# Kernel tuning notes

Measured on AMD Instinct MI355X. Metric: run time of the kernel, lower is better.

Reference implementation:

```python
import jax, jax.numpy as jnp
import numpy as np

B, A, C = 1, 196416, 90
H = W = 1024
SCORE_THRESHOLD = 0.05
MAX_DETECTIONS = 100
# RetinaNet-style BBoxTransform normalization (mean=0, std=[0.1,0.1,0.2,0.2])
STD = (0.1, 0.1, 0.2, 0.2)


def setup_inputs() -> dict:
    key = jax.random.key(0)
    k1, k2, k3, k4, k5, k6, k7 = jax.random.split(key, 7)
    x = jax.random.normal(k1, (B, 3, H, W), dtype=jnp.float32)
    regression = jax.random.normal(k2, (B, A, 4), dtype=jnp.float32) * 0.1
    classification = jax.random.normal(k3, (B, A, C), dtype=jnp.float32)
    # valid anchor boxes (x1, y1, x2, y2)
    cx = jax.random.uniform(k4, (B, A), minval=0.0, maxval=float(W))
    cy = jax.random.uniform(k5, (B, A), minval=0.0, maxval=float(H))
    aw = jax.random.uniform(k6, (B, A), minval=16.0, maxval=256.0)
    ah = jax.random.uniform(k7, (B, A), minval=16.0, maxval=256.0)
    anchors = jnp.stack([cx - 0.5 * aw, cy - 0.5 * ah, cx + 0.5 * aw, cy + 0.5 * ah], axis=2).astype(jnp.float32)
    return {"x": x, "regression": regression, "classification": classification, "anchors": anchors}


def _decode_clip(anchors, regression, img_h, img_w):
    # BBoxTransform: deltas (dx, dy, dw, dh) scaled by std, applied to anchor center/size
    wa = anchors[..., 2] - anchors[..., 0]
    ha = anchors[..., 3] - anchors[..., 1]
    cxa = anchors[..., 0] + 0.5 * wa
    cya = anchors[..., 1] + 0.5 * ha
    dx = regression[..., 0] * STD[0]
    dy = regression[..., 1] * STD[1]
    dw = regression[..., 2] * STD[2]
    dh = regression[..., 3] * STD[3]
    cx = cxa + dx * wa
    cy = cya + dy * ha
    w = jnp.exp(dw) * wa
    h = jnp.exp(dh) * ha
    # ClipBoxes: x1,y1 clamped at 0; x2,y2 clamped at image width/height
    x1 = jnp.maximum(cx - 0.5 * w, 0.0)
    y1 = jnp.maximum(cy - 0.5 * h, 0.0)
    x2 = jnp.minimum(cx + 0.5 * w, float(img_w))
    y2 = jnp.minimum(cy + 0.5 * h, float(img_h))
    return jnp.stack([x1, y1, x2, y2], axis=2)  # [B, A, 4]


def reference(x, regression, classification, anchors):
    img_h, img_w = x.shape[2], x.shape[3]
    boxes = _decode_clip(anchors, regression, img_h, img_w)  # [1, A, 4]
    probs = jax.nn.sigmoid(classification)                    # [1, A, C]
    scores = jnp.max(probs, axis=2)                           # [1, A]
    classes = jnp.argmax(probs, axis=2)                       # [1, A]
    valid_scores = jnp.where(scores > SCORE_THRESHOLD, scores, 0.0)
    vb = boxes[0]            # [A, 4]
    vc = classes[0]          # [A]
    vs = valid_scores[0]     # [A]
    k = min(MAX_DETECTIONS, vs.shape[0])
    _, top_idx = jax.lax.top_k(vs, k)
    final_boxes = vb[top_idx]
    final_scores = vs[top_idx]
    final_classes = vc[top_idx]
    return (final_boxes, final_scores, final_classes)
```

## Files before the change

### kernel.cpp

```cpp
#include <hip/hip_runtime.h>
#include <cmath>

#define A_CNT 196416
#define C_CNT 90
#define QUADS (A_CNT / 4)
#define QITERS (QUADS / 8)
#define TOPK 100u
#define CAPB 2048
#define NB_RED 1536
#define NB_GAT 192

#define OFF_HIST1 785664u
#define OFF_CTRL  789760u
#define OFF_CANDA 789824u
#define OFF_CANDB 790336u

#define AGENT_LD(p)    __hip_atomic_load((p), __ATOMIC_RELAXED, __HIP_MEMORY_SCOPE_AGENT)
#define AGENT_ST(p, v) __hip_atomic_store((p), (v), __ATOMIC_RELAXED, __HIP_MEMORY_SCOPE_AGENT)

__global__ __launch_bounds__(256, 4) void k_reduce(const float* __restrict__ cls,
                                                   unsigned* __restrict__ keys,
                                                   unsigned* __restrict__ hist1,
                                                   unsigned* __restrict__ ctrl) {
    __shared__ unsigned lhist[576];
    __shared__ unsigned sdata[256];
    __shared__ unsigned sbin[2];
    __shared__ int sflag;
    const int t = threadIdx.x;
    for (int j = t; j < 576; j += 256) lhist[j] = 0u;
    __syncthreads();

    const int lane = t & 63;
    const int g = lane >> 3, s = lane & 7;
    const int wid = blockIdx.x * 4 + (t >> 6);
    const float4* __restrict__ cls4 = (const float4*)cls;

    if (wid < QITERS) {
        const int q = wid * 8 + g;
        const float4* __restrict__ r4 = cls4 + (size_t)q * 90;
        float4 v[12];
#pragma unroll
        for (int i = 0; i < 12; ++i) {
            const int j = s + 8 * i;
            v[i] = r4[(j < 90) ? j : 89];
        }
        float m0 = -INFINITY, m1 = -INFINITY, m2 = -INFINITY, m3 = -INFINITY;
#pragma unroll
        for (int i = 0; i < 12; ++i) {
            const int j = s + 8 * i;
            const float4 vv = v[i];
            const float a01 = fmaxf(vv.x, vv.y), a23 = fmaxf(vv.z, vv.w);
            const float all = fmaxf(a01, a23);
            if (j < 22)       m0 = fmaxf(m0, all);
            else if (j == 22) { m0 = fmaxf(m0, a01); m1 = fmaxf(m1, a23); }
            else if (j < 45)  m1 = fmaxf(m1, all);
            else if (j < 67)  m2 = fmaxf(m2, all);
            else if (j == 67) { m2 = fmaxf(m2, a01); m3 = fmaxf(m3, a23); }
            else if (j < 90)  m3 = fmaxf(m3, all);
        }
#pragma unroll
        for (int d = 1; d < 8; d <<= 1) {
            m0 = fmaxf(m0, __shfl_xor(m0, d));
            m1 = fmaxf(m1, __shfl_xor(m1, d));
            m2 = fmaxf(m2, __shfl_xor(m2, d));
            m3 = fmaxf(m3, __shfl_xor(m3, d));
        }
        if (s == 0) {
            float p0 = 1.0f / (1.0f + expf(-m0));
            float p1 = 1.0f / (1.0f + expf(-m1));
            float p2 = 1.0f / (1.0f + expf(-m2));
            float p3 = 1.0f / (1.0f + expf(-m3));
            unsigned k0 = (p0 > 0.05f) ? __float_as_uint(p0) : 0u;
            unsigned k1 = (p1 > 0.05f) ? __float_as_uint(p1) : 0u;
            unsigned k2 = (p2 > 0.05f) ? __float_as_uint(p2) : 0u;
            unsigned k3 = (p3 > 0.05f) ? __float_as_uint(p3) : 0u;
            *(uint4*)(keys + 4 * (size_t)q) = make_uint4(k0, k1, k2, k3);
            unsigned h0 = k0 ? (min(k0 >> 16, 0x3F80u) - 0x3D4Bu) : 0u;
            unsigned h1 = k1 ? (min(k1 >> 16, 0x3F80u) - 0x3D4Bu) : 0u;
            unsigned h2 = k2 ? (min(k2 >> 16, 0x3F80u) - 0x3D4Bu) : 0u;
            unsigned h3 = k3 ? (min(k3 >> 16, 0x3F80u) - 0x3D4Bu) : 0u;
            atomicAdd(&lhist[h0], 1u);
            atomicAdd(&lhist[h1], 1u);
            atomicAdd(&lhist[h2], 1u);
            atomicAdd(&lhist[h3], 1u);
        }
    }
    __syncthreads();
    for (int j = t; j < 576; j += 256) {
        unsigned c = lhist[j];
        if (c) atomicAdd(&hist1[j], c);
    }
    __syncthreads();
    if (t == 0) sflag = (atomicAdd(&ctrl[8], 1u) == NB_RED - 1u) ? 1 : 0;
    __syncthreads();
    if (!sflag) return;

    const unsigned target = TOPK;
    unsigned ssum = 0;
#pragma unroll
    for (int j = 0; j < 4; ++j) ssum += AGENT_LD(&hist1[t * 4 + j]);
    sdata[t] = ssum;
    for (int d = 1; d < 256; d <<= 1) {
        __syncthreads();
        unsigned add = (t + d < 256) ? sdata[t + d] : 0u;
        __syncthreads();
        sdata[t] += add;
    }
    __syncthreads();
    {
        unsigned mysuf  = sdata[t];
        unsigned nxtsuf = (t < 255) ? sdata[t + 1] : 0u;
        if (nxtsuf < target && mysuf >= target) { sbin[0] = (unsigned)t; sbin[1] = nxtsuf; }
    }
    __syncthreads();
    const unsigned chunkB = sbin[0];
    const unsigned gAbove = sbin[1];
    unsigned v = (t < 4) ? AGENT_LD(&hist1[chunkB * 4 + t]) : 0u;
    sdata[t] = v;
    for (int d = 1; d < 256; d <<= 1) {
        __syncthreads();
        unsigned add = (t + d < 256) ? sdata[t + d] : 0u;
        __syncthreads();
        sdata[t] += add;
    }
    __syncthreads();
    {
        unsigned mysuf  = sdata[t] + gAbove;
        unsigned nxtsuf = ((t < 255) ? sdata[t + 1] : 0u) + gAbove;
        if (nxtsuf < target && mysuf >= target) {
            unsigned bin = chunkB * 4 + (unsigned)t;
            ctrl[0] = bin ? (bin + 0x3D4Bu) : 0u;
            ctrl[1] = nxtsuf;
        }
    }
}

__global__ __launch_bounds__(256) void k_gather(const float* __restrict__ cls,
                                                const float* __restrict__ reg,
                                                const float* __restrict__ anc,
                                                const unsigned* __restrict__ keys,
                                                unsigned* __restrict__ ctrl,
                                                unsigned* __restrict__ candA,
                                                unsigned* __restrict__ candB,
                                                float* __restrict__ out) {
    __shared__ unsigned sAi[128], sAk[128];
    __shared__ unsigned sBi[CAPB], sBk[CAPB];
    __shared__ unsigned sel[TOPK];
    __shared__ int sflag;
    const int t = threadIdx.x;

    const unsigned binB = ctrl[0];
    const int i4 = blockIdx.x * 256 + t;
    if (i4 < A_CNT / 4) {
        uint4 k = ((const uint4*)keys)[i4];
        const unsigned base = (unsigned)(4 * i4);
#pragma unroll
        for (int j = 0; j < 4; ++j) {
            unsigned kk = (j == 0) ? k.x : (j == 1) ? k.y : (j == 2) ? k.z : k.w;
            unsigned t16 = kk >> 16;
            if (t16 > binB) {
                unsigned q = atomicAdd(&ctrl[5], 1u);
                if (q < 128u) AGENT_ST(&candA[q], base + j);
            } else if (t16 == binB) {
                unsigned q = atomicAdd(&ctrl[6], 1u);
                if (q < (unsigned)CAPB) AGENT_ST(&candB[q], base + j);
            }
        }
    }
    __syncthreads();
    if (t == 0) sflag = (atomicAdd(&ctrl[9], 1u) == (unsigned)NB_GAT - 1u) ? 1 : 0;
    __syncthreads();
    if (!sflag) return;

    const unsigned nA = min(AGENT_LD(&ctrl[5]), 128u);
    const unsigned nB = min(AGENT_LD(&ctrl[6]), (unsigned)CAPB);
    const unsigned need = TOPK - nA;

    if (t < (int)nA) { unsigned i = AGENT_LD(&candA[t]); sAi[t] = i; sAk[t] = keys[i]; }
    for (unsigned e = (unsigned)t; e < nB; e += 256u) {
        unsigned i = AGENT_LD(&candB[e]); sBi[e] = i; sBk[e] = keys[i];
    }
    __syncthreads();

    if (t < (int)nA) {
        unsigned mi = sAi[t], mk = sAk[t], r = 0;
        for (unsigned j = 0; j < nA; ++j) {
            unsigned ok = sAk[j];
            if (ok > mk || (ok == mk && sAi[j] < mi)) r++;
        }
        sel[r] = mi;
    }
    for (unsigned e = (unsigned)t; e < nB; e += 256u) {
        unsigned mi = sBi[e], mk = sBk[e], r = 0;
        for (unsigned j = 0; j < nB; ++j) {
            unsigned ok = sBk[j];
            if (ok > mk || (ok == mk && sBi[j] < mi)) r++;
        }
        if (r < need) sel[nA + r] = mi;
    }
    __syncthreads();

    if (t < (int)TOPK) {
        const unsigned a = sel[t];
        const float2* __restrict__ row = (const float2*)(cls + (size_t)a * C_CNT);
        float2 vr[45];
#pragma unroll
        for (int c = 0; c < 45; ++c) vr[c] = row[c];
        float bv = -INFINITY; int bi = 0;
#pragma unroll
        for (int c = 0; c < 45; ++c) {
            if (vr[c].x > bv) { bv = vr[c].x; bi = 2 * c; }
            if (vr[c].y > bv) { bv = vr[c].y; bi = 2 * c + 1; }
        }
        float score = __uint_as_float(keys[a]);
        const float4 an = ((const float4*)anc)[a];
        const float4 rg = ((const float4*)reg)[a];
        float wa = an.z - an.x, ha = an.w - an.y;
        float cxa = an.x + 0.5f * wa, cya = an.y + 0.5f * ha;
        float dx = rg.x * 0.1f, dy = rg.y * 0.1f;
        float dw = rg.z * 0.2f, dh = rg.w * 0.2f;
        float cx = cxa + dx * wa, cy = cya + dy * ha;
        float w = expf(dw) * wa, h = expf(dh) * ha;
        out[t * 4 + 0] = fmaxf(cx - 0.5f * w, 0.0f);
        out[t * 4 + 1] = fmaxf(cy - 0.5f * h, 0.0f);
        out[t * 4 + 2] = fminf(cx + 0.5f * w, 1024.0f);
        out[t * 4 + 3] = fminf(cy + 0.5f * h, 1024.0f);
        out[400 + t] = score;
        out[500 + t] = (float)bi;
    }
}

extern "C" void kernel_launch(void* const* d_in, const int* in_sizes, int n_in,
                              void* d_out, int out_size, void* d_ws, size_t ws_size,
                              hipStream_t stream) {
    const float* reg = (const float*)d_in[1];
    const float* cls = (const float*)d_in[2];
    const float* anc = (const float*)d_in[3];
    float* out = (float*)d_out;
    char* ws = (char*)d_ws;
    unsigned* keys  = (unsigned*)ws;
    unsigned* hist1 = (unsigned*)(ws + OFF_HIST1);
    unsigned* ctrl  = (unsigned*)(ws + OFF_CTRL);
    unsigned* candA = (unsigned*)(ws + OFF_CANDA);
    unsigned* candB = (unsigned*)(ws + OFF_CANDB);

    hipMemsetAsync(hist1, 0, 4096 + 64, stream);
    k_reduce<<<NB_RED, 256, 0, stream>>>(cls, keys, hist1, ctrl);
    k_gather<<<NB_GAT, 256, 0, stream>>>(cls, reg, anc, keys, ctrl, candA, candB, out);
}
```

Before: 146.6 us.

## Process three quad-groups per wave with double-buffered register loads in k_reduce

The reduce kernel launches a third as many blocks (512 instead of 1536). Each wave now handles up to three quad-iterations with a software pipeline: it loads the next row group into a second register buffer while reducing the current one, and sched barriers keep loads issued early. The goal is to keep more loads in flight per wave and cut block launch and per-block histogram flush and atomic overhead. In exchange, register use doubles, and launch bounds drop to 2 blocks per SM, which lowers occupancy.

```diff
diff --git a/kernel.cpp b/kernel.cpp
--- a/kernel.cpp
+++ b/kernel.cpp
@@ -7,7 +7,8 @@
 #define QITERS (QUADS / 8)
 #define TOPK 100u
 #define CAPB 2048
-#define NB_RED 1536
+#define NB_RED 512
+#define NWAVES 2048
 #define NB_GAT 192
 
 #define OFF_HIST1 785664u
@@ -18,7 +19,63 @@
 #define AGENT_LD(p)    __hip_atomic_load((p), __ATOMIC_RELAXED, __HIP_MEMORY_SCOPE_AGENT)
 #define AGENT_ST(p, v) __hip_atomic_store((p), (v), __ATOMIC_RELAXED, __HIP_MEMORY_SCOPE_AGENT)
 
-__global__ __launch_bounds__(256, 4) void k_reduce(const float* __restrict__ cls,
+
+#define LOADQ(V, qq)                                                        \
+    {                                                                       \
+        const float4* __restrict__ r4_ = cls4 + (size_t)(qq) * 90;          \
+        _Pragma("unroll")                                                   \
+        for (int i_ = 0; i_ < 12; ++i_) {                                   \
+            const int j_ = s + 8 * i_;                                      \
+            V[i_] = r4_[(j_ < 90) ? j_ : 89];   \
+        }                                                                   \
+    }                                                                       \
+    __builtin_amdgcn_sched_barrier(0);
+
+#define REDUCE_EMIT(V, qq)                                                  \
+    {                                                                       \
+        float m0 = -INFINITY, m1 = -INFINITY, m2 = -INFINITY, m3 = -INFINITY; \
+        _Pragma("unroll")                                                   \
+        for (int i_ = 0; i_ < 12; ++i_) {                                   \
+            const int j_ = s + 8 * i_;                                      \
+            const float4 vv = V[i_];                                        \
+            const float a01 = fmaxf(vv.x, vv.y), a23 = fmaxf(vv.z, vv.w);   \
+            const float all = fmaxf(a01, a23);                              \
+            if (j_ < 22)       m0 = fmaxf(m0, all);                         \
+            else if (j_ == 22) { m0 = fmaxf(m0, a01); m1 = fmaxf(m1, a23); }\
+            else if (j_ < 45)  m1 = fmaxf(m1, all);                         \
+            else if (j_ < 67)  m2 = fmaxf(m2, all);                         \
+            else if (j_ == 67) { m2 = fmaxf(m2, a01); m3 = fmaxf(m3, a23); }\
+            else if (j_ < 90)  m3 = fmaxf(m3, all);                         \
+        }                                                                   \
+        _Pragma("unroll")                                                   \
+        for (int d_ = 1; d_ < 8; d_ <<= 1) {                                \
+            m0 = fmaxf(m0, __shfl_xor(m0, d_));                             \
+            m1 = fmaxf(m1, __shfl_xor(m1, d_));                             \
+            m2 = fmaxf(m2, __shfl_xor(m2, d_));                             \
+            m3 = fmaxf(m3, __shfl_xor(m3, d_));                             \
+        }                                                                   \
+        if (s == 0) {                                                       \
+            float p0 = 1.0f / (1.0f + expf(-m0));    \
+            float p1 = 1.0f / (1.0f + expf(-m1));                           \
+            float p2 = 1.0f / (1.0f + expf(-m2));                           \
+            float p3 = 1.0f / (1.0f + expf(-m3));                           \
+            unsigned k0 = (p0 > 0.05f) ? __float_as_uint(p0) : 0u;          \
+            unsigned k1 = (p1 > 0.05f) ? __float_as_uint(p1) : 0u;          \
+            unsigned k2 = (p2 > 0.05f) ? __float_as_uint(p2) : 0u;          \
+            unsigned k3 = (p3 > 0.05f) ? __float_as_uint(p3) : 0u;          \
+            *(uint4*)(keys + 4 * (size_t)(qq)) = make_uint4(k0, k1, k2, k3);\
+            unsigned h0 = k0 ? (min(k0 >> 16, 0x3F80u) - 0x3D4Bu) : 0u;     \
+            unsigned h1 = k1 ? (min(k1 >> 16, 0x3F80u) - 0x3D4Bu) : 0u;     \
+            unsigned h2 = k2 ? (min(k2 >> 16, 0x3F80u) - 0x3D4Bu) : 0u;     \
+            unsigned h3 = k3 ? (min(k3 >> 16, 0x3F80u) - 0x3D4Bu) : 0u;     \
+            atomicAdd(&lhist[h0], 1u);                                      \
+            atomicAdd(&lhist[h1], 1u);                                      \
+            atomicAdd(&lhist[h2], 1u);                                      \
+            atomicAdd(&lhist[h3], 1u);                                      \
+        }                                                                   \
+    }
+
+__global__ __launch_bounds__(256, 2) void k_reduce(const float* __restrict__ cls,
                                                    unsigned* __restrict__ keys,
                                                    unsigned* __restrict__ hist1,
                                                    unsigned* __restrict__ ctrl) {
@@ -32,59 +89,25 @@
 
     const int lane = t & 63;
     const int g = lane >> 3, s = lane & 7;
-    const int wid = blockIdx.x * 4 + (t >> 6);
+    const int w = blockIdx.x * 4 + (t >> 6);
     const float4* __restrict__ cls4 = (const float4*)cls;
 
-    if (wid < QITERS) {
-        const int q = wid * 8 + g;
-        const float4* __restrict__ r4 = cls4 + (size_t)q * 90;
-        float4 v[12];
-#pragma unroll
-        for (int i = 0; i < 12; ++i) {
-            const int j = s + 8 * i;
-            v[i] = r4[(j < 90) ? j : 89];
-        }
-        float m0 = -INFINITY, m1 = -INFINITY, m2 = -INFINITY, m3 = -INFINITY;
-#pragma unroll
-        for (int i = 0; i < 12; ++i) {
-            const int j = s + 8 * i;
-            const float4 vv = v[i];
-            const float a01 = fmaxf(vv.x, vv.y), a23 = fmaxf(vv.z, vv.w);
-            const float all = fmaxf(a01, a23);
-            if (j < 22)       m0 = fmaxf(m0, all);
-            else if (j == 22) { m0 = fmaxf(m0, a01); m1 = fmaxf(m1, a23); }
-            else if (j < 45)  m1 = fmaxf(m1, all);
-            else if (j < 67)  m2 = fmaxf(m2, all);
-            else if (j == 67) { m2 = fmaxf(m2, a01); m3 = fmaxf(m3, a23); }
-            else if (j < 90)  m3 = fmaxf(m3, all);
-        }
-#pragma unroll
-        for (int d = 1; d < 8; d <<= 1) {
-            m0 = fmaxf(m0, __shfl_xor(m0, d));
-            m1 = fmaxf(m1, __shfl_xor(m1, d));
-            m2 = fmaxf(m2, __shfl_xor(m2, d));
-            m3 = fmaxf(m3, __shfl_xor(m3, d));
-        }
-        if (s == 0) {
-            float p0 = 1.0f / (1.0f + expf(-m0));
-            float p1 = 1.0f / (1.0f + expf(-m1));
-            float p2 = 1.0f / (1.0f + expf(-m2));
-            float p3 = 1.0f / (1.0f + expf(-m3));
-            unsigned k0 = (p0 > 0.05f) ? __float_as_uint(p0) : 0u;
-            unsigned k1 = (p1 > 0.05f) ? __float_as_uint(p1) : 0u;
-            unsigned k2 = (p2 > 0.05f) ? __float_as_uint(p2) : 0u;
-            unsigned k3 = (p3 > 0.05f) ? __float_as_uint(p3) : 0u;
-            *(uint4*)(keys + 4 * (size_t)q) = make_uint4(k0, k1, k2, k3);
-            unsigned h0 = k0 ? (min(k0 >> 16, 0x3F80u) - 0x3D4Bu) : 0u;
-            unsigned h1 = k1 ? (min(k1 >> 16, 0x3F80u) - 0x3D4Bu) : 0u;
-            unsigned h2 = k2 ? (min(k2 >> 16, 0x3F80u) - 0x3D4Bu) : 0u;
-            unsigned h3 = k3 ? (min(k3 >> 16, 0x3F80u) - 0x3D4Bu) : 0u;
-            atomicAdd(&lhist[h0], 1u);
-            atomicAdd(&lhist[h1], 1u);
-            atomicAdd(&lhist[h2], 1u);
-            atomicAdd(&lhist[h3], 1u);
-        }
-    }
+    const int qi0 = w;
+    const int qi1 = w + NWAVES;
+    const int qi2 = w + 2 * NWAVES;
+    const bool has2 = (qi2 < QITERS);
+    const int q0 = qi0 * 8 + g;
+    const int q1 = qi1 * 8 + g;
+    const int q2 = (has2 ? qi2 : qi0) * 8 + g;
+
+    float4 vA[12], vB[12];
+    LOADQ(vA, q0);
+    LOADQ(vB, q1);
+    REDUCE_EMIT(vA, q0);
+    LOADQ(vA, q2);
+    REDUCE_EMIT(vB, q1);
+    if (has2) REDUCE_EMIT(vA, q2);
+
     __syncthreads();
     for (int j = t; j < 576; j += 256) {
         unsigned c = lhist[j];
```

Result: faster. 133.9 us (-8.7%).
